# Optimization experiments

Measured on AMD Instinct MI355X. Metric: run time of the kernel, lower is better.

Reference implementation:

```python
import jax, jax.numpy as jnp
import numpy as np

D_MODEL = 2048
N_HEADS = 16
D_K = D_MODEL // N_HEADS


def setup_inputs() -> dict:
    key = jax.random.key(0)
    ks = jax.random.split(key, 9)
    s = 1.0 / np.sqrt(D_MODEL)
    def lin(k):
        kw, kb = jax.random.split(k)
        W = jax.random.uniform(kw, (D_MODEL, D_MODEL), jnp.float32, -s, s)
        b = jax.random.uniform(kb, (D_MODEL,), jnp.float32, -s, s)
        return W, b
    Wq, bq = lin(ks[0])
    Wk, bk = lin(ks[1])
    Wv, bv = lin(ks[2])
    Wo, bo = lin(ks[3])
    x = jax.random.normal(ks[4], (2, 2048, D_MODEL), jnp.float32)
    return {"x": x, "Wq": Wq, "bq": bq, "Wk": Wk, "bk": bk,
            "Wv": Wv, "bv": bv, "Wo": Wo, "bo": bo}


def _mha(x, Wq, bq, Wk, bk, Wv, bv, Wo, bo):
    B, S, _ = x.shape
    # Linear projections (torch Linear: x @ W.T + b), split into heads: b s (h d) -> b h s d
    def proj(W, b):
        y = jnp.einsum('bsm,nm->bsn', x, W) + b
        return y.reshape(B, S, N_HEADS, D_K).transpose(0, 2, 1, 3)
    q = proj(Wq, bq)
    k = proj(Wk, bk)
    v = proj(Wv, bv)
    scores = jnp.einsum('bhsd,bhtd->bhst', q, k) / jnp.sqrt(jnp.float32(D_K))
    causal = jnp.triu(jnp.ones((S, S), bool), k=1)  # True above diagonal -> masked
    scores = jnp.where(causal[None, None], -jnp.inf, scores)
    attn = jax.nn.softmax(scores, axis=-1)  # dropout p=0 (eval)
    out = jnp.einsum('bhst,bhtd->bhsd', attn, v)
    out = out.transpose(0, 2, 1, 3).reshape(B, S, D_MODEL)
    return jnp.einsum('bsm,nm->bsn', out, Wo) + bo


def reference(x, Wq, bq, Wk, bk, Wv, bv, Wo, bo):
    return _mha(x, Wq, bq, Wk, bk, Wv, bv, Wo, bo)
```

## Files before the change

### kernel.cpp

```cpp
#include <hip/hip_runtime.h>

typedef unsigned short u16;
typedef __attribute__((ext_vector_type(8))) short bf16x8;
typedef __attribute__((ext_vector_type(4))) float f32x4;
typedef __attribute__((ext_vector_type(4))) unsigned short u16x4;

__device__ __forceinline__ u16 f2bf(float f) {
  union { float f; unsigned u; } v; v.f = f;
  return (u16)((v.u + 0x7FFFu + ((v.u >> 16) & 1u)) >> 16);
}

__device__ __forceinline__ void gload16(const u16* g, u16* l) {
  __builtin_amdgcn_global_load_lds((const __attribute__((address_space(1))) void*)g,
                                   (__attribute__((address_space(3))) void*)l, 16, 0, 0);
}

__global__ __launch_bounds__(256) void k_f2bf5(
    const float* __restrict__ i0, const float* __restrict__ i1, const float* __restrict__ i2,
    const float* __restrict__ i3, const float* __restrict__ i4,
    u16* o0, u16* o1, u16* o2, u16* o3, u16* o4, int n4x, int n4w) {
  const int seg = blockIdx.y;
  const float* in = (seg == 0) ? i0 : (seg == 1) ? i1 : (seg == 2) ? i2 : (seg == 3) ? i3 : i4;
  u16* out = (seg == 0) ? o0 : (seg == 1) ? o1 : (seg == 2) ? o2 : (seg == 3) ? o3 : o4;
  const int n4 = (seg == 0) ? n4x : n4w;
  int i = blockIdx.x * 256 + threadIdx.x;
  const int stride = gridDim.x * 256;
  for (; i < n4; i += stride) {
    const float4 v = ((const float4*)in)[i];
    u16x4 o;
    o.x = f2bf(v.x); o.y = f2bf(v.y); o.z = f2bf(v.z); o.w = f2bf(v.w);
    ((u16x4*)out)[i] = o;
  }
}

template <int OUT_F32>
__global__ __launch_bounds__(256, 4) void k_gemm12(
    const u16* __restrict__ A, const u16* __restrict__ Bt,
    const float* __restrict__ b0, const float* __restrict__ b1, const float* __restrict__ b2,
    u16* __restrict__ C0, u16* __restrict__ C1, u16* __restrict__ C2,
    float* __restrict__ Cf, int NBM)
{
  __shared__ alignas(16) u16 As[8192];
  __shared__ alignas(16) u16 Bs[8192];

  const int tid = threadIdx.x;
  const int lane = tid & 63, wid = tid >> 6;
  const int fr = lane & 15, fg = lane >> 4;
  const int wr = wid >> 1, wc = wid & 1;

  const int nblk = gridDim.x;
  const int q = nblk >> 3, r = nblk & 7;
  const int xcd = blockIdx.x & 7, lid = blockIdx.x >> 3;
  const int wgid = (xcd < r ? xcd * (q + 1) : r * (q + 1) + (xcd - r) * q) + lid;
  const int mb = wgid % NBM, nb = wgid / NBM;
  const long row0 = (long)mb * 128;
  const long col0 = (long)nb * 128;

  int sRow[4], sCol[4];
#pragma unroll
  for (int i = 0; i < 4; ++i) {
    const int g = (wid * 4 + i) * 64 + lane;
    sRow[i] = g >> 3;
    sCol[i] = ((g & 7) ^ (sRow[i] & 7)) << 3;
  }

  const int sw = fr & 7;
  const int aBase = (wr * 64 + fr) * 64;
  const int bBase = (wc * 64 + fr) * 64;
  const int pc0 = (fg ^ sw) << 3;
  const int pc1 = ((4 + fg) ^ sw) << 3;

  f32x4 acc[4][4] = {};

#pragma unroll 1
  for (int t = 0; t < 32; ++t) {
    if (t) __syncthreads();
    const long k0 = (long)t << 6;
#pragma unroll
    for (int i = 0; i < 4; ++i) {
      gload16(A  + (row0 + sRow[i]) * 2048L + k0 + sCol[i], &As[(wid * 4 + i) * 512]);
      gload16(Bt + (col0 + sRow[i]) * 2048L + k0 + sCol[i], &Bs[(wid * 4 + i) * 512]);
    }
    __syncthreads();

#pragma unroll
    for (int kc = 0; kc < 2; ++kc) {
      const int pc = kc ? pc1 : pc0;
      bf16x8 a[4], b[4];
#pragma unroll
      for (int i = 0; i < 4; ++i) {
        a[i] = *(const bf16x8*)&As[aBase + i * 1024 + pc];
        b[i] = *(const bf16x8*)&Bs[bBase + i * 1024 + pc];
      }
#pragma unroll
      for (int i = 0; i < 4; ++i)
#pragma unroll
        for (int j = 0; j < 4; ++j)
          acc[i][j] = __builtin_amdgcn_mfma_f32_16x16x32_bf16(a[i], b[j], acc[i][j], 0, 0, 0);
    }
  }

  const int seg = (int)(col0 >> 11);
  const long colL = col0 & 2047;
  const float* bp = (seg == 0) ? b0 : (seg == 1) ? b1 : b2;
  u16* Cb = (seg == 0) ? C0 : (seg == 1) ? C1 : C2;
#pragma unroll
  for (int j = 0; j < 4; ++j) {
    const long cN = colL + wc * 64 + j * 16 + fr;
    const float bv = bp[cN];
#pragma unroll
    for (int i = 0; i < 4; ++i) {
      const long rM = row0 + wr * 64 + i * 16 + fg * 4;
#pragma unroll
      for (int reg = 0; reg < 4; ++reg) {
        const float v = acc[i][j][reg] + bv;
        if (OUT_F32) Cf[(rM + reg) * 2048 + cN] = v;
        else         Cb[(rM + reg) * 2048 + cN] = f2bf(v);
      }
    }
  }
}

__global__ __launch_bounds__(256) void k_transpose_v(const u16* __restrict__ V,
                                                     u16* __restrict__ Vt) {
  __shared__ u16 t[64][68];
  const int bh = blockIdx.z;
  const long s0 = (long)blockIdx.x * 64;
  const long d0 = (long)blockIdx.y * 64;
  const int tid = threadIdx.x;
  const long rowbase = (long)(bh >> 4) * 2048;
  const int hcol = (bh & 15) * 128;
#pragma unroll
  for (int i = 0; i < 4; ++i) {
    const int v = tid + i * 256;
    const int r = v >> 4, c4 = (v & 15) << 2;
    const u16x4 val = *(const u16x4*)&V[(rowbase + s0 + r) * 2048 + hcol + d0 + c4];
    *(u16x4*)&t[r][c4] = val;
  }
  __syncthreads();
#pragma unroll
  for (int i = 0; i < 4; ++i) {
    const int v = tid + i * 256;
    const int dr = v >> 4, s4 = (v & 15) << 2;
    u16x4 o;
    o.x = t[s4 + 0][dr]; o.y = t[s4 + 1][dr]; o.z = t[s4 + 2][dr]; o.w = t[s4 + 3][dr];
    *(u16x4*)&Vt[((long)bh * 128 + d0 + dr) * 2048 + s0 + s4] = o;
  }
}

__global__ __launch_bounds__(256, 2) void k_flash_attn(
    const u16* __restrict__ Q, const u16* __restrict__ K, const u16* __restrict__ Vt,
    u16* __restrict__ O)
{
  __shared__ alignas(16) u16 SM[38400];
  u16* Kt  = SM;
  u16* Vtt = SM + 16384;
  u16* Pl  = SM + 32768;
  float* statsM = (float*)(SM + 37888);
  float* statsL = (float*)(SM + 38144);
  float* mergeO = (float*)SM;

  const int tid = threadIdx.x;
  const int lane = tid & 63, wid = tid >> 6;
  const int fr = lane & 15, fg = lane >> 4;
  const int kvh = wid >> 1, qh = wid & 1;

  const int L = blockIdx.x;
  const int bh = (L & 7) * 4 + ((L >> 3) & 3);
  const int bx = L >> 5;

  const long rowbase = (long)(bh >> 4) * 2048;
  const int hcol = (bh & 15) * 128;
  const u16* Kg = K + rowbase * 2048 + hcol;
  const u16* Vg = Vt + (long)bh * 128 * 2048;
  const float scale2 = 0.08838834764831845f * 1.44269504089f;

  int kR[4], kC[4], vR[4], vC[4];
#pragma unroll
  for (int i = 0; i < 4; ++i) {
    const int g = (wid * 4 + i) * 64 + lane;
    kR[i] = g >> 4;
    kC[i] = ((g & 15) ^ (kR[i] & 7)) << 3;
    vR[i] = g >> 3;
    vC[i] = ((g & 7) ^ (vR[i] & 7)) << 3;
  }

  const int sw = fr & 7;
  int kOff[2][4];
#pragma unroll
  for (int kvt = 0; kvt < 2; ++kvt)
#pragma unroll
    for (int c = 0; c < 4; ++c)
      kOff[kvt][c] = kvh * 4096 + kvt * 2048 + fr * 128 + (((c * 4 + fg) ^ sw) << 3);
  const int vB = fr * 64 + (((kvh * 4 + fg) ^ sw) << 3);
  const int pBase = wid * 1280;

  for (int pass = 0; pass < 2; ++pass) {
    const int qblk = pass ? (31 - bx) : bx;
    const int n = qblk + 1;
    const int qw = qblk * 64 + qh * 32;

    bf16x8 qf[2][4];
#pragma unroll
    for (int qs = 0; qs < 2; ++qs)
#pragma unroll
      for (int c = 0; c < 4; ++c)
        qf[qs][c] = *(const bf16x8*)&Q[(rowbase + qw + qs * 16 + fr) * 2048 + hcol + c * 32 + fg * 8];

    f32x4 oacc[2][8] = {};
    float m_run[2] = {-1e30f, -1e30f}, l_run[2] = {0.0f, 0.0f};

#pragma unroll
    for (int i = 0; i < 4; ++i) {
      gload16(Kg + (long)kR[i] * 2048 + kC[i], &Kt[(wid * 4 + i) * 512]);
      gload16(Vg + (long)vR[i] * 2048 + vC[i], &Vtt[(wid * 4 + i) * 512]);
    }

    int cur = 0;
    for (int j = 0; j < n; ++j) {
      if (j + 1 < n) {
        const long kv = (long)(j + 1) * 64;
#pragma unroll
        for (int i = 0; i < 4; ++i) {
          gload16(Kg + (kv + kR[i]) * 2048 + kC[i], &Kt[(cur ^ 1) * 8192 + (wid * 4 + i) * 512]);
          gload16(Vg + (long)vR[i] * 2048 + kv + vC[i], &Vtt[(cur ^ 1) * 8192 + (wid * 4 + i) * 512]);
        }
        asm volatile("s_waitcnt vmcnt(8)" ::: "memory");
      } else {
        asm volatile("s_waitcnt vmcnt(0)" ::: "memory");
      }
      __builtin_amdgcn_s_barrier();
      __builtin_amdgcn_sched_barrier(0);

      const int kvbase = j * 64 + kvh * 32;
      const bool skip = (kvbase >= qw + 32);
      if (!skip) {
        const bool needmask = (kvbase + 31 > qw);

        f32x4 st[2][2] = {};
        const u16* kt = &Kt[cur * 8192];
        __builtin_amdgcn_s_setprio(1);
#pragma unroll
        for (int kvt = 0; kvt < 2; ++kvt)
#pragma unroll
          for (int c = 0; c < 4; ++c) {
            const bf16x8 kf = *(const bf16x8*)&kt[kOff[kvt][c]];
            st[0][kvt] = __builtin_amdgcn_mfma_f32_16x16x32_bf16(kf, qf[0][c], st[0][kvt], 0, 0, 0);
            st[1][kvt] = __builtin_amdgcn_mfma_f32_16x16x32_bf16(kf, qf[1][c], st[1][kvt], 0, 0, 0);
          }
        __builtin_amdgcn_s_setprio(0);

        float pmax[2] = {-1e30f, -1e30f};
        if (needmask) {
#pragma unroll
          for (int qs = 0; qs < 2; ++qs) {
            const int qg = qw + qs * 16 + fr;
#pragma unroll
            for (int kvt = 0; kvt < 2; ++kvt)
#pragma unroll
              for (int r = 0; r < 4; ++r) {
                const int kg = kvbase + kvt * 16 + fg * 4 + r;
                const float v = (kg <= qg) ? st[qs][kvt][r] * scale2 : -1e30f;
                st[qs][kvt][r] = v;
                pmax[qs] = fmaxf(pmax[qs], v);
              }
          }
        } else {
#pragma unroll
          for (int qs = 0; qs < 2; ++qs)
#pragma unroll
            for (int kvt = 0; kvt < 2; ++kvt)
#pragma unroll
              for (int r = 0; r < 4; ++r) {
                const float v = st[qs][kvt][r] * scale2;
                st[qs][kvt][r] = v;
                pmax[qs] = fmaxf(pmax[qs], v);
              }
        }
#pragma unroll
        for (int qs = 0; qs < 2; ++qs) {
          pmax[qs] = fmaxf(pmax[qs], __shfl_xor(pmax[qs], 16));
          pmax[qs] = fmaxf(pmax[qs], __shfl_xor(pmax[qs], 32));
        }

        const int ok = (pmax[0] <= m_run[0] + 8.f) & (pmax[1] <= m_run[1] + 8.f);
        if (!__all(ok)) {
#pragma unroll
          for (int qs = 0; qs < 2; ++qs) {
            const float nm = fmaxf(m_run[qs], pmax[qs]);
            const float al = exp2f(m_run[qs] - nm);
            l_run[qs] *= al;
            m_run[qs] = nm;
#pragma unroll
            for (int dt = 0; dt < 8; ++dt)
#pragma unroll
              for (int r = 0; r < 4; ++r) oacc[qs][dt][r] *= al;
          }
        }

        float lsum[2] = {0.f, 0.f};
#pragma unroll
        for (int qs = 0; qs < 2; ++qs)
#pragma unroll
          for (int kvt = 0; kvt < 2; ++kvt)
#pragma unroll
            for (int r = 0; r < 4; ++r) {
              const float p = exp2f(st[qs][kvt][r] - m_run[qs]);
              st[qs][kvt][r] = p;
              lsum[qs] += p;
            }
#pragma unroll
        for (int qs = 0; qs < 2; ++qs) {
          lsum[qs] += __shfl_xor(lsum[qs], 16);
          lsum[qs] += __shfl_xor(lsum[qs], 32);
          l_run[qs] += lsum[qs];
        }

#pragma unroll
        for (int qs = 0; qs < 2; ++qs)
#pragma unroll
          for (int kvt = 0; kvt < 2; ++kvt)
#pragma unroll
            for (int r = 0; r < 4; ++r)
              Pl[pBase + (qs * 16 + fr) * 40 + kvt * 16 + fg * 4 + r] = f2bf(st[qs][kvt][r]);
        asm volatile("s_waitcnt lgkmcnt(0)" ::: "memory");
        __builtin_amdgcn_sched_barrier(0);

        const u16* vt = &Vtt[cur * 8192];
        const bf16x8 pf0 = *(const bf16x8*)&Pl[pBase + fr * 40 + fg * 8];
        const bf16x8 pf1 = *(const bf16x8*)&Pl[pBase + (16 + fr) * 40 + fg * 8];
        __builtin_amdgcn_s_setprio(1);
#pragma unroll
        for (int dt = 0; dt < 8; ++dt) {
          const bf16x8 vf = *(const bf16x8*)&vt[vB + dt * 1024];
          oacc[0][dt] = __builtin_amdgcn_mfma_f32_16x16x32_bf16(vf, pf0, oacc[0][dt], 0, 0, 0);
          oacc[1][dt] = __builtin_amdgcn_mfma_f32_16x16x32_bf16(vf, pf1, oacc[1][dt], 0, 0, 0);
        }
        __builtin_amdgcn_s_setprio(0);
      }

      asm volatile("" ::: "memory");
      __builtin_amdgcn_s_barrier();
      cur ^= 1;
    }

    if (fg == 0) {
#pragma unroll
      for (int qs = 0; qs < 2; ++qs) {
        statsM[wid * 32 + qs * 16 + fr] = m_run[qs];
        statsL[wid * 32 + qs * 16 + fr] = l_run[qs];
      }
    }
    __syncthreads();
    const int pw = wid ^ 2;
    float aself[2], ltot[2];
#pragma unroll
    for (int qs = 0; qs < 2; ++qs) {
      const float mp = statsM[pw * 32 + qs * 16 + fr];
      const float lp = statsL[pw * 32 + qs * 16 + fr];
      const float m = fmaxf(m_run[qs], mp);
      aself[qs] = exp2f(m_run[qs] - m);
      const float ap = exp2f(mp - m);
      ltot[qs] = aself[qs] * l_run[qs] + ap * lp;
    }
    if (kvh == 1) {
#pragma unroll
      for (int qs = 0; qs < 2; ++qs)
#pragma unroll
        for (int dt = 0; dt < 8; ++dt)
#pragma unroll
          for (int r = 0; r < 4; ++r)
            mergeO[qh * 4224 + (qs * 16 + fr) * 132 + dt * 16 + fg * 4 + r] =
                aself[qs] * oacc[qs][dt][r];
    }
    __syncthreads();
    if (kvh == 0) {
#pragma unroll
      for (int qs = 0; qs < 2; ++qs) {
        const float inv = 1.0f / ltot[qs];
        const long orow = (rowbase + qw + qs * 16 + fr) * 2048 + hcol;
#pragma unroll
        for (int dt = 0; dt < 8; ++dt) {
          u16x4 o;
#pragma unroll
          for (int r = 0; r < 4; ++r)
            o[r] = f2bf((aself[qs] * oacc[qs][dt][r] +
                         mergeO[qh * 4224 + (qs * 16 + fr) * 132 + dt * 16 + fg * 4 + r]) * inv);
          *(u16x4*)&O[orow + dt * 16 + fg * 4] = o;
        }
      }
    }
    __syncthreads();
  }
}

extern "C" void kernel_launch(void* const* d_in, const int* in_sizes, int n_in,
                              void* d_out, int out_size, void* d_ws, size_t ws_size,
                              hipStream_t stream) {
  const float* x  = (const float*)d_in[0];
  const float* Wq = (const float*)d_in[1];
  const float* bq = (const float*)d_in[2];
  const float* Wk = (const float*)d_in[3];
  const float* bk = (const float*)d_in[4];
  const float* Wv = (const float*)d_in[5];
  const float* bv = (const float*)d_in[6];
  const float* Wo = (const float*)d_in[7];
  const float* bo = (const float*)d_in[8];
  float* out = (float*)d_out;

  char* ws = (char*)d_ws;
  const size_t SZ_X = 16777216;
  const size_t SZ_W = 8388608;
  u16* xb  = (u16*)(ws);
  u16* wqb = (u16*)(ws + SZ_X);
  u16* wkb = (u16*)(ws + SZ_X + 1 * SZ_W);
  u16* wvb = (u16*)(ws + SZ_X + 2 * SZ_W);
  u16* wob = (u16*)(ws + SZ_X + 3 * SZ_W);
  u16* Qb  = (u16*)(ws + 1 * SZ_X + 4 * SZ_W);
  u16* Kb  = (u16*)(ws + 2 * SZ_X + 4 * SZ_W);
  u16* Vb  = (u16*)(ws + 3 * SZ_X + 4 * SZ_W);
  u16* Vtb = (u16*)(ws + 4 * SZ_X + 4 * SZ_W);
  u16* Ob  = Vb;

  k_f2bf5<<<dim3(1024, 5), 256, 0, stream>>>(x, Wq, Wk, Wv, Wo,
                                             xb, wqb, wkb, wvb, wob,
                                             8388608 / 4, 4194304 / 4);

  k_gemm12<0><<<1536, 256, 0, stream>>>(xb, wqb, bq, bk, bv, Qb, Kb, Vb, nullptr, 32);

  k_transpose_v<<<dim3(32, 2, 32), 256, 0, stream>>>(Vb, Vtb);

  k_flash_attn<<<512, 256, 0, stream>>>(Qb, Kb, Vtb, Ob);

  k_gemm12<1><<<512, 256, 0, stream>>>(Ob, wob, bo, bo, bo, nullptr, nullptr, nullptr, out, 32);
}
```

Measured before the change: 260.1 us.

## Drop double-buffered KV prefetch and launch one query block per workgroup

The causal flash-attention kernel no longer pairs a light and a heavy query block in two passes per workgroup. It now launches 1024 workgroups, one query block each, ordered heaviest first. The K/V LDS double buffer becomes a single buffer loaded synchronously with barriers, which shrinks LDS and raises the launch bound to 3 blocks per CU so more waves can hide latency. In exchange, load/compute overlap inside a workgroup is lost, and the balanced work pairing now depends on the hardware scheduler.

```diff
diff --git a/kernel.cpp b/kernel.cpp
--- a/kernel.cpp
+++ b/kernel.cpp
@@ -148,16 +148,16 @@
   }
 }
 
-__global__ __launch_bounds__(256, 2) void k_flash_attn(
+__global__ __launch_bounds__(256, 3) void k_flash_attn(
     const u16* __restrict__ Q, const u16* __restrict__ K, const u16* __restrict__ Vt,
     u16* __restrict__ O)
 {
-  __shared__ alignas(16) u16 SM[38400];
+  __shared__ alignas(16) u16 SM[22016];
   u16* Kt  = SM;
-  u16* Vtt = SM + 16384;
-  u16* Pl  = SM + 32768;
-  float* statsM = (float*)(SM + 37888);
-  float* statsL = (float*)(SM + 38144);
+  u16* Vtt = SM + 8192;
+  u16* Pl  = SM + 16384;
+  float* statsM = (float*)(SM + 21504);
+  float* statsL = (float*)(SM + 21760);
   float* mergeO = (float*)SM;
 
   const int tid = threadIdx.x;
@@ -167,7 +167,7 @@
 
   const int L = blockIdx.x;
   const int bh = (L & 7) * 4 + ((L >> 3) & 3);
-  const int bx = L >> 5;
+  const int qblk = 31 - (L >> 5);
 
   const long rowbase = (long)(bh >> 4) * 2048;
   const int hcol = (bh & 15) * 128;
@@ -195,202 +195,181 @@
   const int vB = fr * 64 + (((kvh * 4 + fg) ^ sw) << 3);
   const int pBase = wid * 1280;
 
-  for (int pass = 0; pass < 2; ++pass) {
-    const int qblk = pass ? (31 - bx) : bx;
-    const int n = qblk + 1;
-    const int qw = qblk * 64 + qh * 32;
-
-    bf16x8 qf[2][4];
+  const int n = qblk + 1;
+  const int qw = qblk * 64 + qh * 32;
+
+  bf16x8 qf[2][4];
+#pragma unroll
+  for (int qs = 0; qs < 2; ++qs)
+#pragma unroll
+    for (int c = 0; c < 4; ++c)
+      qf[qs][c] = *(const bf16x8*)&Q[(rowbase + qw + qs * 16 + fr) * 2048 + hcol + c * 32 + fg * 8];
+
+  f32x4 oacc[2][8] = {};
+  float m_run[2] = {-1e30f, -1e30f}, l_run[2] = {0.0f, 0.0f};
+
+  for (int j = 0; j < n; ++j) {
+    if (j) __syncthreads();
+    const long kv = (long)j * 64;
+#pragma unroll
+    for (int i = 0; i < 4; ++i) {
+      gload16(Kg + (kv + kR[i]) * 2048 + kC[i], &Kt[(wid * 4 + i) * 512]);
+      gload16(Vg + (long)vR[i] * 2048 + kv + vC[i], &Vtt[(wid * 4 + i) * 512]);
+    }
+    __syncthreads();
+
+    const int kvbase = j * 64 + kvh * 32;
+    const bool skip = (kvbase >= qw + 32);
+    if (!skip) {
+      const bool needmask = (kvbase + 31 > qw);
+
+      f32x4 st[2][2] = {};
+      __builtin_amdgcn_s_setprio(1);
+#pragma unroll
+      for (int kvt = 0; kvt < 2; ++kvt)
+#pragma unroll
+        for (int c = 0; c < 4; ++c) {
+          const bf16x8 kf = *(const bf16x8*)&Kt[kOff[kvt][c]];
+          st[0][kvt] = __builtin_amdgcn_mfma_f32_16x16x32_bf16(kf, qf[0][c], st[0][kvt], 0, 0, 0);
+          st[1][kvt] = __builtin_amdgcn_mfma_f32_16x16x32_bf16(kf, qf[1][c], st[1][kvt], 0, 0, 0);
+        }
+      __builtin_amdgcn_s_setprio(0);
+
+      float pmax[2] = {-1e30f, -1e30f};
+      if (needmask) {
+#pragma unroll
+        for (int qs = 0; qs < 2; ++qs) {
+          const int qg = qw + qs * 16 + fr;
+#pragma unroll
+          for (int kvt = 0; kvt < 2; ++kvt)
+#pragma unroll
+            for (int r = 0; r < 4; ++r) {
+              const int kg = kvbase + kvt * 16 + fg * 4 + r;
+              const float v = (kg <= qg) ? st[qs][kvt][r] * scale2 : -1e30f;
+              st[qs][kvt][r] = v;
+              pmax[qs] = fmaxf(pmax[qs], v);
+            }
+        }
+      } else {
+#pragma unroll
+        for (int qs = 0; qs < 2; ++qs)
+#pragma unroll
+          for (int kvt = 0; kvt < 2; ++kvt)
+#pragma unroll
+            for (int r = 0; r < 4; ++r) {
+              const float v = st[qs][kvt][r] * scale2;
+              st[qs][kvt][r] = v;
+              pmax[qs] = fmaxf(pmax[qs], v);
+            }
+      }
+#pragma unroll
+      for (int qs = 0; qs < 2; ++qs) {
+        pmax[qs] = fmaxf(pmax[qs], __shfl_xor(pmax[qs], 16));
+        pmax[qs] = fmaxf(pmax[qs], __shfl_xor(pmax[qs], 32));
+      }
+
+      const int ok = (pmax[0] <= m_run[0] + 8.f) & (pmax[1] <= m_run[1] + 8.f);
+      if (!__all(ok)) {
+#pragma unroll
+        for (int qs = 0; qs < 2; ++qs) {
+          const float nm = fmaxf(m_run[qs], pmax[qs]);
+          const float al = exp2f(m_run[qs] - nm);
+          l_run[qs] *= al;
+          m_run[qs] = nm;
+#pragma unroll
+          for (int dt = 0; dt < 8; ++dt)
+#pragma unroll
+            for (int r = 0; r < 4; ++r) oacc[qs][dt][r] *= al;
+        }
+      }
+
+      float lsum[2] = {0.f, 0.f};
+#pragma unroll
+      for (int qs = 0; qs < 2; ++qs)
+#pragma unroll
+        for (int kvt = 0; kvt < 2; ++kvt)
+#pragma unroll
+          for (int r = 0; r < 4; ++r) {
+            const float p = exp2f(st[qs][kvt][r] - m_run[qs]);
+            st[qs][kvt][r] = p;
+            lsum[qs] += p;
+          }
+#pragma unroll
+      for (int qs = 0; qs < 2; ++qs) {
+        lsum[qs] += __shfl_xor(lsum[qs], 16);
+        lsum[qs] += __shfl_xor(lsum[qs], 32);
+        l_run[qs] += lsum[qs];
+      }
+
+#pragma unroll
+      for (int qs = 0; qs < 2; ++qs)
+#pragma unroll
+        for (int kvt = 0; kvt < 2; ++kvt)
+#pragma unroll
+          for (int r = 0; r < 4; ++r)
+            Pl[pBase + (qs * 16 + fr) * 40 + kvt * 16 + fg * 4 + r] = f2bf(st[qs][kvt][r]);
+      asm volatile("s_waitcnt lgkmcnt(0)" ::: "memory");
+      __builtin_amdgcn_sched_barrier(0);
+
+      const bf16x8 pf0 = *(const bf16x8*)&Pl[pBase + fr * 40 + fg * 8];
+      const bf16x8 pf1 = *(const bf16x8*)&Pl[pBase + (16 + fr) * 40 + fg * 8];
+      __builtin_amdgcn_s_setprio(1);
+#pragma unroll
+      for (int dt = 0; dt < 8; ++dt) {
+        const bf16x8 vf = *(const bf16x8*)&Vtt[vB + dt * 1024];
+        oacc[0][dt] = __builtin_amdgcn_mfma_f32_16x16x32_bf16(vf, pf0, oacc[0][dt], 0, 0, 0);
+        oacc[1][dt] = __builtin_amdgcn_mfma_f32_16x16x32_bf16(vf, pf1, oacc[1][dt], 0, 0, 0);
+      }
+      __builtin_amdgcn_s_setprio(0);
+    }
+  }
+
+  __syncthreads();
+  if (fg == 0) {
+#pragma unroll
+    for (int qs = 0; qs < 2; ++qs) {
+      statsM[wid * 32 + qs * 16 + fr] = m_run[qs];
+      statsL[wid * 32 + qs * 16 + fr] = l_run[qs];
+    }
+  }
+  __syncthreads();
+  const int pw = wid ^ 2;
+  float aself[2], ltot[2];
+#pragma unroll
+  for (int qs = 0; qs < 2; ++qs) {
+    const float mp = statsM[pw * 32 + qs * 16 + fr];
+    const float lp = statsL[pw * 32 + qs * 16 + fr];
+    const float m = fmaxf(m_run[qs], mp);
+    aself[qs] = exp2f(m_run[qs] - m);
+    const float ap = exp2f(mp - m);
+    ltot[qs] = aself[qs] * l_run[qs] + ap * lp;
+  }
+  if (kvh == 1) {
 #pragma unroll
     for (int qs = 0; qs < 2; ++qs)
 #pragma unroll
-      for (int c = 0; c < 4; ++c)
-        qf[qs][c] = *(const bf16x8*)&Q[(rowbase + qw + qs * 16 + fr) * 2048 + hcol + c * 32 + fg * 8];
-
-    f32x4 oacc[2][8] = {};
-    float m_run[2] = {-1e30f, -1e30f}, l_run[2] = {0.0f, 0.0f};
-
-#pragma unroll
-    for (int i = 0; i < 4; ++i) {
-      gload16(Kg + (long)kR[i] * 2048 + kC[i], &Kt[(wid * 4 + i) * 512]);
-      gload16(Vg + (long)vR[i] * 2048 + vC[i], &Vtt[(wid * 4 + i) * 512]);
-    }
-
-    int cur = 0;
-    for (int j = 0; j < n; ++j) {
-      if (j + 1 < n) {
-        const long kv = (long)(j + 1) * 64;
-#pragma unroll
-        for (int i = 0; i < 4; ++i) {
-          gload16(Kg + (kv + kR[i]) * 2048 + kC[i], &Kt[(cur ^ 1) * 8192 + (wid * 4 + i) * 512]);
-          gload16(Vg + (long)vR[i] * 2048 + kv + vC[i], &Vtt[(cur ^ 1) * 8192 + (wid * 4 + i) * 512]);
-        }
-        asm volatile("s_waitcnt vmcnt(8)" ::: "memory");
-      } else {
-        asm volatile("s_waitcnt vmcnt(0)" ::: "memory");
-      }
-      __builtin_amdgcn_s_barrier();
-      __builtin_amdgcn_sched_barrier(0);
-
-      const int kvbase = j * 64 + kvh * 32;
-      const bool skip = (kvbase >= qw + 32);
-      if (!skip) {
-        const bool needmask = (kvbase + 31 > qw);
-
-        f32x4 st[2][2] = {};
-        const u16* kt = &Kt[cur * 8192];
-        __builtin_amdgcn_s_setprio(1);
-#pragma unroll
-        for (int kvt = 0; kvt < 2; ++kvt)
-#pragma unroll
-          for (int c = 0; c < 4; ++c) {
-            const bf16x8 kf = *(const bf16x8*)&kt[kOff[kvt][c]];
-            st[0][kvt] = __builtin_amdgcn_mfma_f32_16x16x32_bf16(kf, qf[0][c], st[0][kvt], 0, 0, 0);
-            st[1][kvt] = __builtin_amdgcn_mfma_f32_16x16x32_bf16(kf, qf[1][c], st[1][kvt], 0, 0, 0);
-          }
-        __builtin_amdgcn_s_setprio(0);
-
-        float pmax[2] = {-1e30f, -1e30f};
-        if (needmask) {
-#pragma unroll
-          for (int qs = 0; qs < 2; ++qs) {
-            const int qg = qw + qs * 16 + fr;
-#pragma unroll
-            for (int kvt = 0; kvt < 2; ++kvt)
-#pragma unroll
-              for (int r = 0; r < 4; ++r) {
-                const int kg = kvbase + kvt * 16 + fg * 4 + r;
-                const float v = (kg <= qg) ? st[qs][kvt][r] * scale2 : -1e30f;
-                st[qs][kvt][r] = v;
-                pmax[qs] = fmaxf(pmax[qs], v);
-              }
-          }
-        } else {
-#pragma unroll
-          for (int qs = 0; qs < 2; ++qs)
-#pragma unroll
-            for (int kvt = 0; kvt < 2; ++kvt)
-#pragma unroll
-              for (int r = 0; r < 4; ++r) {
-                const float v = st[qs][kvt][r] * scale2;
-                st[qs][kvt][r] = v;
-                pmax[qs] = fmaxf(pmax[qs], v);
-              }
-        }
-#pragma unroll
-        for (int qs = 0; qs < 2; ++qs) {
-          pmax[qs] = fmaxf(pmax[qs], __shfl_xor(pmax[qs], 16));
-          pmax[qs] = fmaxf(pmax[qs], __shfl_xor(pmax[qs], 32));
-        }
-
-        const int ok = (pmax[0] <= m_run[0] + 8.f) & (pmax[1] <= m_run[1] + 8.f);
-        if (!__all(ok)) {
-#pragma unroll
-          for (int qs = 0; qs < 2; ++qs) {
-            const float nm = fmaxf(m_run[qs], pmax[qs]);
-            const float al = exp2f(m_run[qs] - nm);
-            l_run[qs] *= al;
-            m_run[qs] = nm;
-#pragma unroll
-            for (int dt = 0; dt < 8; ++dt)
-#pragma unroll
-              for (int r = 0; r < 4; ++r) oacc[qs][dt][r] *= al;
-          }
-        }
-
-        float lsum[2] = {0.f, 0.f};
-#pragma unroll
-        for (int qs = 0; qs < 2; ++qs)
-#pragma unroll
-          for (int kvt = 0; kvt < 2; ++kvt)
-#pragma unroll
-            for (int r = 0; r < 4; ++r) {
-              const float p = exp2f(st[qs][kvt][r] - m_run[qs]);
-              st[qs][kvt][r] = p;
-              lsum[qs] += p;
-            }
-#pragma unroll
-        for (int qs = 0; qs < 2; ++qs) {
-          lsum[qs] += __shfl_xor(lsum[qs], 16);
-          lsum[qs] += __shfl_xor(lsum[qs], 32);
-          l_run[qs] += lsum[qs];
-        }
-
-#pragma unroll
-        for (int qs = 0; qs < 2; ++qs)
-#pragma unroll
-          for (int kvt = 0; kvt < 2; ++kvt)
-#pragma unroll
-            for (int r = 0; r < 4; ++r)
-              Pl[pBase + (qs * 16 + fr) * 40 + kvt * 16 + fg * 4 + r] = f2bf(st[qs][kvt][r]);
-        asm volatile("s_waitcnt lgkmcnt(0)" ::: "memory");
-        __builtin_amdgcn_sched_barrier(0);
-
-        const u16* vt = &Vtt[cur * 8192];
-        const bf16x8 pf0 = *(const bf16x8*)&Pl[pBase + fr * 40 + fg * 8];
-        const bf16x8 pf1 = *(const bf16x8*)&Pl[pBase + (16 + fr) * 40 + fg * 8];
-        __builtin_amdgcn_s_setprio(1);
-#pragma unroll
-        for (int dt = 0; dt < 8; ++dt) {
-          const bf16x8 vf = *(const bf16x8*)&vt[vB + dt * 1024];
-          oacc[0][dt] = __builtin_amdgcn_mfma_f32_16x16x32_bf16(vf, pf0, oacc[0][dt], 0, 0, 0);
-          oacc[1][dt] = __builtin_amdgcn_mfma_f32_16x16x32_bf16(vf, pf1, oacc[1][dt], 0, 0, 0);
-        }
-        __builtin_amdgcn_s_setprio(0);
-      }
-
-      asm volatile("" ::: "memory");
-      __builtin_amdgcn_s_barrier();
-      cur ^= 1;
-    }
-
-    if (fg == 0) {
-#pragma unroll
-      for (int qs = 0; qs < 2; ++qs) {
-        statsM[wid * 32 + qs * 16 + fr] = m_run[qs];
-        statsL[wid * 32 + qs * 16 + fr] = l_run[qs];
-      }
-    }
-    __syncthreads();
-    const int pw = wid ^ 2;
-    float aself[2], ltot[2];
+      for (int dt = 0; dt < 8; ++dt)
+#pragma unroll
+        for (int r = 0; r < 4; ++r)
+          mergeO[qh * 4224 + (qs * 16 + fr) * 132 + dt * 16 + fg * 4 + r] =
+              aself[qs] * oacc[qs][dt][r];
+  }
+  __syncthreads();
+  if (kvh == 0) {
 #pragma unroll
     for (int qs = 0; qs < 2; ++qs) {
-      const float mp = statsM[pw * 32 + qs * 16 + fr];
-      const float lp = statsL[pw * 32 + qs * 16 + fr];
-      const float m = fmaxf(m_run[qs], mp);
-      aself[qs] = exp2f(m_run[qs] - m);
-      const float ap = exp2f(mp - m);
-      ltot[qs] = aself[qs] * l_run[qs] + ap * lp;
-    }
-    if (kvh == 1) {
-#pragma unroll
-      for (int qs = 0; qs < 2; ++qs)
-#pragma unroll
-        for (int dt = 0; dt < 8; ++dt)
-#pragma unroll
-          for (int r = 0; r < 4; ++r)
-            mergeO[qh * 4224 + (qs * 16 + fr) * 132 + dt * 16 + fg * 4 + r] =
-                aself[qs] * oacc[qs][dt][r];
-    }
-    __syncthreads();
-    if (kvh == 0) {
-#pragma unroll
-      for (int qs = 0; qs < 2; ++qs) {
-        const float inv = 1.0f / ltot[qs];
-        const long orow = (rowbase + qw + qs * 16 + fr) * 2048 + hcol;
-#pragma unroll
-        for (int dt = 0; dt < 8; ++dt) {
-          u16x4 o;
-#pragma unroll
-          for (int r = 0; r < 4; ++r)
-            o[r] = f2bf((aself[qs] * oacc[qs][dt][r] +
-                         mergeO[qh * 4224 + (qs * 16 + fr) * 132 + dt * 16 + fg * 4 + r]) * inv);
-          *(u16x4*)&O[orow + dt * 16 + fg * 4] = o;
-        }
-      }
-    }
-    __syncthreads();
+      const float inv = 1.0f / ltot[qs];
+      const long orow = (rowbase + qw + qs * 16 + fr) * 2048 + hcol;
+#pragma unroll
+      for (int dt = 0; dt < 8; ++dt) {
+        u16x4 o;
+#pragma unroll
+        for (int r = 0; r < 4; ++r)
+          o[r] = f2bf((aself[qs] * oacc[qs][dt][r] +
+                       mergeO[qh * 4224 + (qs * 16 + fr) * 132 + dt * 16 + fg * 4 + r]) * inv);
+        *(u16x4*)&O[orow + dt * 16 + fg * 4] = o;
+      }
+    }
   }
 }
 
@@ -430,7 +409,7 @@
 
   k_transpose_v<<<dim3(32, 2, 32), 256, 0, stream>>>(Vb, Vtb);
 
-  k_flash_attn<<<512, 256, 0, stream>>>(Qb, Kb, Vtb, Ob);
+  k_flash_attn<<<1024, 256, 0, stream>>>(Qb, Kb, Vtb, Ob);
 
   k_gemm12<1><<<512, 256, 0, stream>>>(Ob, wob, bo, bo, bo, nullptr, nullptr, nullptr, out, 32);
 }
```

Measured after the change: 284.7 us. 1.09x slower.
